# Kernel optimization log

Measured on AMD Instinct MI355X. Metric: run time of the kernel, lower is better.

The kernel has to match this reference:

```python
import jax, jax.numpy as jnp
import numpy as np

PATCH_SIDE = 20  # hardcoded in GenericCamera.project


def _resize_ac(img, out_h, out_w):
    """Bilinear resize with align_corners=True, matching F.interpolate. img: (B,C,H,W)."""
    B, C, H, W = img.shape
    ys = jnp.arange(out_h, dtype=jnp.float32) * (np.float32(H - 1) / np.float32(out_h - 1))
    xs = jnp.arange(out_w, dtype=jnp.float32) * (np.float32(W - 1) / np.float32(out_w - 1))
    y0 = jnp.floor(ys).astype(jnp.int32); y1 = jnp.minimum(y0 + 1, H - 1)
    x0 = jnp.floor(xs).astype(jnp.int32); x1 = jnp.minimum(x0 + 1, W - 1)
    wy = (ys - y0.astype(jnp.float32)).astype(img.dtype)
    wx = (xs - x0.astype(jnp.float32)).astype(img.dtype)
    top = img[:, :, y0, :] * (1 - wy)[None, None, :, None] + img[:, :, y1, :] * wy[None, None, :, None]
    return top[:, :, :, x0] * (1 - wx) + top[:, :, :, x1] * wx


def setup_inputs() -> dict:
    key = jax.random.key(0)
    k1, k2 = jax.random.split(key)
    B, H, W = 1, 128, 416
    R = jax.random.normal(k1, (B, 3, H, W), dtype=jnp.float32)
    X = jax.random.normal(k2, (B, 3, H, W), dtype=jnp.float32)
    return {"R": R, "X": X, "progress": 10}


def reference(R, X, progress):
    B, C, H_full, W_full = X.shape
    kh = PATCH_SIDE
    Ks = 2 * kh + 1          # 41
    K = Ks * Ks              # 1681
    H, W = H_full // 2, W_full // 2  # downsample=True

    ray = _resize_ac(R, H, W)          # (1,3,H,W)
    direction = _resize_ac(X, H, W)    # (1,3,H,W)

    # clamped patch window start per row/col (boundary shift logic of _get_patch_coords)
    sx = jnp.clip(jnp.arange(H) - kh, 0, H - 1 - 2 * kh)   # (H,)
    sy = jnp.clip(jnp.arange(W) - kh, 0, W - 1 - 2 * kh)   # (W,)
    off = jnp.arange(Ks)
    cx = sx[:, None] + off[None, :]    # (H,41) row indices of patch
    cy = sy[:, None] + off[None, :]    # (W,41) col indices of patch

    # separable patch gather: (3,H,W) -> (3,H,41,W) -> (3,H,41,W,41)
    r = ray[0]
    patch = r[:, cx, :][:, :, :, cy]                       # (3,H,41,W,41)
    patch = patch.transpose(0, 1, 3, 2, 4).reshape(3, H * W, K)  # (3,N,K)

    dirn = direction.reshape(B, 3, H * W)
    dirn = dirn / jnp.linalg.norm(dirn, axis=1, keepdims=True)
    d = dirn[0]                                            # (3,N)

    logits = jnp.einsum('cn,cnk->nk', d, patch)            # (N,K)
    temperature = np.float32(max(1e-8, 1e-4 / np.exp(0.1 * float(progress))))
    sm = jax.nn.softmax(logits / temperature, axis=-1)     # (N,K)

    # soft-argmax over patch coordinates (coords stored as (x,y) = (row,col))
    px = jnp.broadcast_to(cx[:, None, :, None], (H, W, Ks, Ks)).reshape(H * W, K).astype(jnp.float32)
    py = jnp.broadcast_to(cy[None, :, None, :], (H, W, Ks, Ks)).reshape(H * W, K).astype(jnp.float32)
    ix = jnp.einsum('nk,nk->n', sm, px).reshape(H, W)
    iy = jnp.einsum('nk,nk->n', sm, py).reshape(H, W)

    Xn = 2.0 * ix / (H - 1) - 1.0
    Yn = 2.0 * iy / (W - 1) - 1.0
    Xn = _resize_ac(Xn[None, None], H_full, W_full)[0, 0]
    Yn = _resize_ac(Yn[None, None], H_full, W_full)[0, 0]
    return jnp.stack([Yn, Xn], axis=-1).reshape(B, H_full, W_full, 2)
```

## Files before the change

kernel.cpp:

```cpp
#include <hip/hip_runtime.h>
#include <math.h>

#define HS 64
#define WS 208
#define HF 128
#define WF 416
#define NS (HS * WS)
#define KH 20
#define KS 41
#define KK (KS * KS)
#define NJ2 7
#define GRID 2048
#define LOG2E 1.442695040888963f

__device__ __forceinline__ void ac_idx(int o, int inN, float sc, int& i0, int& i1, float& w) {
#pragma clang fp contract(off)
    float s = (float)o * sc;
    float f = floorf(s);
    i0 = (int)f;
    i1 = min(i0 + 1, inN - 1);
    w = s - f;
}

__global__ void k_down(const float* __restrict__ R, const float* __restrict__ X,
                       const int* __restrict__ prog,
                       float4* __restrict__ ray4, float4* __restrict__ dir4,
                       float* __restrict__ tbuf) {
#pragma clang fp contract(off)
    int n = blockIdx.x * blockDim.x + threadIdx.x;
    if (n >= NS) return;
    if (n == 0) {
        double T64 = fmax(1e-8, 1e-4 / exp(0.1 * (double)prog[0]));
        tbuf[0] = (float)T64;
    }
    int y = n / WS, x = n - y * WS;
    int y0, y1, x0, x1; float wy, wx;
    ac_idx(y, HF, 127.0f / 63.0f, y0, y1, wy);
    ac_idx(x, WF, 415.0f / 207.0f, x0, x1, wx);
    float omwy = 1.0f - wy, omwx = 1.0f - wx;
    float r[3], d[3];
#pragma unroll
    for (int c = 0; c < 3; ++c) {
        const float* p = R + c * (HF * WF);
        float v00 = p[y0 * WF + x0], v10 = p[y1 * WF + x0];
        float v01 = p[y0 * WF + x1], v11 = p[y1 * WF + x1];
        float a0 = v00 * omwy; float b0 = v10 * wy; float t0 = a0 + b0;
        float a1 = v01 * omwy; float b1 = v11 * wy; float t1 = a1 + b1;
        float c0 = t0 * omwx; float c1 = t1 * wx;
        r[c] = c0 + c1;
        const float* q = X + c * (HF * WF);
        float u00 = q[y0 * WF + x0], u10 = q[y1 * WF + x0];
        float u01 = q[y0 * WF + x1], u11 = q[y1 * WF + x1];
        float e0 = u00 * omwy; float f0 = u10 * wy; float s0 = e0 + f0;
        float e1 = u01 * omwy; float f1 = u11 * wy; float s1 = e1 + f1;
        float g0 = s0 * omwx; float g1 = s1 * wx;
        d[c] = g0 + g1;
    }
    float q0 = d[0] * d[0]; float q1 = d[1] * d[1]; float q2 = d[2] * d[2];
    float ssq = (q0 + q1) + q2;
    float nrm = (float)sqrt((double)ssq);
    ray4[n] = make_float4(r[0], r[1], r[2], 0.0f);
    dir4[n] = make_float4(d[0] / nrm, d[1] / nrm, d[2] / nrm, 0.0f);
}

__global__ __launch_bounds__(256, 6) void k_main(const float4* __restrict__ ray4,
                                                 const float4* __restrict__ dir4,
                                                 const float* __restrict__ tbuf,
                                                 float* __restrict__ xn,
                                                 float* __restrict__ yn) {
#pragma clang fp contract(off)
    int tid = (int)threadIdx.x;
    int lane = tid & 63;
    int wid = tid >> 6;
    int k1i = (tid * 25) >> 10;
    int k2i = tid - k1i * KS;
    float Tf = tbuf[0];

    __shared__ float smax[4];
    __shared__ float ssum[4][3];

    for (int pix = (int)blockIdx.x; pix < NS; pix += GRID) {
        int h = pix / WS, w = pix - h * WS;
        int srow = min(max(h - KH, 0), HS - 1 - 2 * KH);
        int scol = min(max(w - KH, 0), WS - 1 - 2 * KH);

        float4 dv = dir4[pix];
        float d0 = dv.x, d1 = dv.y, d2 = dv.z;

        int off = (srow + k1i) * WS + scol + k2i;
        int colk = k2i;

        float lg[NJ2];
        float m = -INFINITY;
#pragma unroll
        for (int j = 0; j < NJ2 - 1; ++j) {
            float4 v = ray4[off];
            float p0 = d0 * v.x; float p1 = d1 * v.y; float p2 = d2 * v.z;
            float l = (p0 + p1) + p2;
            lg[j] = l;
            m = fmaxf(m, l);
            int cn = colk + 10;
            bool cr = cn >= KS;
            colk = cr ? cn - KS : cn;
            off += cr ? (7 * WS - 31) : (6 * WS + 10);
        }
        {
            float l = -INFINITY;
            if (tid < KK - 256 * (NJ2 - 1)) {
                float4 v = ray4[off];
                float p0 = d0 * v.x; float p1 = d1 * v.y; float p2 = d2 * v.z;
                l = (p0 + p1) + p2;
            }
            lg[NJ2 - 1] = l;
            m = fmaxf(m, l);
        }
#pragma unroll
        for (int s = 1; s < 64; s <<= 1) m = fmaxf(m, __shfl_xor(m, s));

        if (lane == 0) smax[wid] = m;
        __syncthreads();
        m = fmaxf(fmaxf(smax[0], smax[1]), fmaxf(smax[2], smax[3]));

        float zm = m / Tf;
        float thresh = m - 0.004f;

        float se = 0.f, sr = 0.f, sc = 0.f;
        int c1 = k1i, c2 = k2i;
#pragma unroll
        for (int j = 0; j < NJ2; ++j) {
            bool a = lg[j] > thresh;
            if (__ballot(a)) {
                float z = lg[j] / Tf;
                float arg = (z - zm) * LOG2E;
                float e = a ? __builtin_amdgcn_exp2f(arg) : 0.0f;
                se += e;
                sr += e * (float)(srow + c1);
                sc += e * (float)(scol + c2);
            }
            int cn = c2 + 10;
            bool cr = cn >= KS;
            c2 = cr ? cn - KS : cn;
            c1 += cr ? 7 : 6;
        }
#pragma unroll
        for (int s = 1; s < 64; s <<= 1) {
            se += __shfl_xor(se, s);
            sr += __shfl_xor(sr, s);
            sc += __shfl_xor(sc, s);
        }
        if (lane == 0) { ssum[wid][0] = se; ssum[wid][1] = sr; ssum[wid][2] = sc; }
        __syncthreads();
        if (tid == 0) {
            float SE = (ssum[0][0] + ssum[1][0]) + (ssum[2][0] + ssum[3][0]);
            float SR = (ssum[0][1] + ssum[1][1]) + (ssum[2][1] + ssum[3][1]);
            float SC = (ssum[0][2] + ssum[1][2]) + (ssum[2][2] + ssum[3][2]);
            double ix = (double)SR / (double)SE, iy = (double)SC / (double)SE;
            xn[pix] = (float)(2.0 * ix / (double)(HS - 1) - 1.0);
            yn[pix] = (float)(2.0 * iy / (double)(WS - 1) - 1.0);
        }
    }
}

__global__ void k_up(const float* __restrict__ xn, const float* __restrict__ yn,
                     float* __restrict__ out) {
#pragma clang fp contract(off)
    int i = blockIdx.x * blockDim.x + threadIdx.x;
    if (i >= HF * WF) return;
    int hh = i / WF, ww = i - hh * WF;
    int y0, y1, x0, x1; float wy, wx;
    ac_idx(hh, HS, 63.0f / 127.0f, y0, y1, wy);
    ac_idx(ww, WS, 207.0f / 415.0f, x0, x1, wx);
    float omwy = 1.0f - wy, omwx = 1.0f - wx;
    float a0, b0, t0, t1;
    a0 = xn[y0 * WS + x0] * omwy; b0 = xn[y1 * WS + x0] * wy; t0 = a0 + b0;
    a0 = xn[y0 * WS + x1] * omwy; b0 = xn[y1 * WS + x1] * wy; t1 = a0 + b0;
    float bx = t0 * omwx + t1 * wx;
    a0 = yn[y0 * WS + x0] * omwy; b0 = yn[y1 * WS + x0] * wy; t0 = a0 + b0;
    a0 = yn[y0 * WS + x1] * omwy; b0 = yn[y1 * WS + x1] * wy; t1 = a0 + b0;
    float ay = t0 * omwx + t1 * wx;
    out[2 * i]     = ay;
    out[2 * i + 1] = bx;
}

extern "C" void kernel_launch(void* const* d_in, const int* in_sizes, int n_in,
                              void* d_out, int out_size, void* d_ws, size_t ws_size,
                              hipStream_t stream) {
    const float* R = (const float*)d_in[0];
    const float* X = (const float*)d_in[1];
    const int* prog = (const int*)d_in[2];
    float4* ray4 = (float4*)d_ws;
    float4* dir4 = ray4 + NS;
    float* xn   = (float*)(dir4 + NS);
    float* yn   = xn + NS;
    float* tbuf = yn + NS;
    float* out  = (float*)d_out;

    k_down<<<(NS + 255) / 256, 256, 0, stream>>>(R, X, prog, ray4, dir4, tbuf);
    k_main<<<GRID, 256, 0, stream>>>(ray4, dir4, tbuf, xn, yn);
    k_up<<<(HF * WF + 255) / 256, 256, 0, stream>>>(xn, yn, out);
}
```

Baseline: 33.33 us.

## Share a staged LDS patch tile across eight pixels, one wave per pixel

Replaces the per-pixel 256-thread block (grid-stride over pixels) with blocks of 512 threads that handle eight horizontally adjacent pixels of one row. The union of their 41x48 patch window is loaded cooperatively into shared memory once. Each wave then computes one pixel's softmax soft-argmax from LDS with only wave-level shuffles, removing block barriers per pixel and redundant global/L2 reads of overlapping patches. It trades this for 31KB of LDS per block and more serial work per lane (27 elements). The ray buffer is padded because the tile load can read past the end of the array.

```diff
diff --git a/kernel.cpp b/kernel.cpp
--- a/kernel.cpp
+++ b/kernel.cpp
@@ -9,8 +9,10 @@
 #define KH 20
 #define KS 41
 #define KK (KS * KS)
-#define NJ2 7
-#define GRID 2048
+#define TCOL 48
+#define PITCH 49
+#define TEL (KS * TCOL)
+#define NBLK (HS * 26)
 #define LOG2E 1.442695040888963f
 
 __device__ __forceinline__ void ac_idx(int o, int inN, float sc, int& i0, int& i1, float& w) {
@@ -63,101 +65,106 @@
     dir4[n] = make_float4(d[0] / nrm, d[1] / nrm, d[2] / nrm, 0.0f);
 }
 
-__global__ __launch_bounds__(256, 6) void k_main(const float4* __restrict__ ray4,
-                                                 const float4* __restrict__ dir4,
-                                                 const float* __restrict__ tbuf,
-                                                 float* __restrict__ xn,
-                                                 float* __restrict__ yn) {
-#pragma clang fp contract(off)
-    int tid = (int)threadIdx.x;
-    int lane = tid & 63;
-    int wid = tid >> 6;
-    int k1i = (tid * 25) >> 10;
-    int k2i = tid - k1i * KS;
+__global__ __launch_bounds__(512) void k_oct(const float4* __restrict__ ray4,
+                                             const float4* __restrict__ dir4,
+                                             const float* __restrict__ tbuf,
+                                             float* __restrict__ xn,
+                                             float* __restrict__ yn) {
+#pragma clang fp contract(off)
+    __shared__ float4 tile[KS * PITCH];
+    int t = (int)threadIdx.x;
+    int lane = t & 63;
+    int wv = t >> 6;
+    int blk = (int)blockIdx.x;
+    int row = (blk * 2521) >> 16;
+    int grp = blk - row * 26;
+    int w0 = grp * 8;
+    int srow = min(max(row - KH, 0), HS - 1 - 2 * KH);
+    int scol0 = min(max(w0 - KH, 0), WS - 1 - 2 * KH);
+
+    int base = srow * WS + scol0;
+#pragma unroll
+    for (int s = 0; s < 4; ++s) {
+        int e = t + 512 * s;
+        if (e < TEL) {
+            int i = (e * 683) >> 15;
+            int j = e - i * TCOL;
+            tile[i * PITCH + j] = ray4[base + i * WS + j];
+        }
+    }
+    __syncthreads();
+
+    int wpx = w0 + wv;
+    int scolp = min(max(wpx - KH, 0), WS - 1 - 2 * KH);
+    int dJ = scolp - scol0;
+    float4 dv = dir4[row * WS + wpx];
+    float d0 = dv.x, d1 = dv.y, d2 = dv.z;
     float Tf = tbuf[0];
 
-    __shared__ float smax[4];
-    __shared__ float ssum[4][3];
-
-    for (int pix = (int)blockIdx.x; pix < NS; pix += GRID) {
-        int h = pix / WS, w = pix - h * WS;
-        int srow = min(max(h - KH, 0), HS - 1 - 2 * KH);
-        int scol = min(max(w - KH, 0), WS - 1 - 2 * KH);
-
-        float4 dv = dir4[pix];
-        float d0 = dv.x, d1 = dv.y, d2 = dv.z;
-
-        int off = (srow + k1i) * WS + scol + k2i;
-        int colk = k2i;
-
-        float lg[NJ2];
-        float m = -INFINITY;
-#pragma unroll
-        for (int j = 0; j < NJ2 - 1; ++j) {
-            float4 v = ray4[off];
+    int k1i = (lane * 25) >> 10;
+    int k2i = lane - k1i * KS;
+    int loff = k1i * PITCH + dJ + k2i;
+    int colk = k2i;
+
+    float lg[27];
+    float m = -INFINITY;
+#pragma unroll
+    for (int j = 0; j < 26; ++j) {
+        float4 v = tile[loff];
+        float p0 = d0 * v.x; float p1 = d1 * v.y; float p2 = d2 * v.z;
+        float l = (p0 + p1) + p2;
+        lg[j] = l;
+        m = fmaxf(m, l);
+        int cn = colk + 23;
+        bool cr = cn >= KS;
+        colk = cr ? cn - KS : cn;
+        loff += cr ? (2 * PITCH - 18) : (PITCH + 23);
+    }
+    {
+        float l = -INFINITY;
+        if (lane < KK - 64 * 26) {
+            float4 v = tile[loff];
             float p0 = d0 * v.x; float p1 = d1 * v.y; float p2 = d2 * v.z;
-            float l = (p0 + p1) + p2;
-            lg[j] = l;
-            m = fmaxf(m, l);
-            int cn = colk + 10;
-            bool cr = cn >= KS;
-            colk = cr ? cn - KS : cn;
-            off += cr ? (7 * WS - 31) : (6 * WS + 10);
+            l = (p0 + p1) + p2;
         }
-        {
-            float l = -INFINITY;
-            if (tid < KK - 256 * (NJ2 - 1)) {
-                float4 v = ray4[off];
-                float p0 = d0 * v.x; float p1 = d1 * v.y; float p2 = d2 * v.z;
-                l = (p0 + p1) + p2;
-            }
-            lg[NJ2 - 1] = l;
-            m = fmaxf(m, l);
+        lg[26] = l;
+        m = fmaxf(m, l);
+    }
+#pragma unroll
+    for (int s = 1; s < 64; s <<= 1) m = fmaxf(m, __shfl_xor(m, s));
+
+    float zm = m / Tf;
+    float thresh = m - 0.004f;
+
+    float se = 0.f, sr = 0.f, sc = 0.f;
+    int c1 = k1i, c2 = k2i;
+#pragma unroll
+    for (int j = 0; j < 27; ++j) {
+        bool a = lg[j] > thresh;
+        if (__ballot(a)) {
+            float z = lg[j] / Tf;
+            float arg = (z - zm) * LOG2E;
+            float e = a ? __builtin_amdgcn_exp2f(arg) : 0.0f;
+            se += e;
+            sr += e * (float)(srow + c1);
+            sc += e * (float)(scolp + c2);
         }
-#pragma unroll
-        for (int s = 1; s < 64; s <<= 1) m = fmaxf(m, __shfl_xor(m, s));
-
-        if (lane == 0) smax[wid] = m;
-        __syncthreads();
-        m = fmaxf(fmaxf(smax[0], smax[1]), fmaxf(smax[2], smax[3]));
-
-        float zm = m / Tf;
-        float thresh = m - 0.004f;
-
-        float se = 0.f, sr = 0.f, sc = 0.f;
-        int c1 = k1i, c2 = k2i;
-#pragma unroll
-        for (int j = 0; j < NJ2; ++j) {
-            bool a = lg[j] > thresh;
-            if (__ballot(a)) {
-                float z = lg[j] / Tf;
-                float arg = (z - zm) * LOG2E;
-                float e = a ? __builtin_amdgcn_exp2f(arg) : 0.0f;
-                se += e;
-                sr += e * (float)(srow + c1);
-                sc += e * (float)(scol + c2);
-            }
-            int cn = c2 + 10;
-            bool cr = cn >= KS;
-            c2 = cr ? cn - KS : cn;
-            c1 += cr ? 7 : 6;
-        }
-#pragma unroll
-        for (int s = 1; s < 64; s <<= 1) {
-            se += __shfl_xor(se, s);
-            sr += __shfl_xor(sr, s);
-            sc += __shfl_xor(sc, s);
-        }
-        if (lane == 0) { ssum[wid][0] = se; ssum[wid][1] = sr; ssum[wid][2] = sc; }
-        __syncthreads();
-        if (tid == 0) {
-            float SE = (ssum[0][0] + ssum[1][0]) + (ssum[2][0] + ssum[3][0]);
-            float SR = (ssum[0][1] + ssum[1][1]) + (ssum[2][1] + ssum[3][1]);
-            float SC = (ssum[0][2] + ssum[1][2]) + (ssum[2][2] + ssum[3][2]);
-            double ix = (double)SR / (double)SE, iy = (double)SC / (double)SE;
-            xn[pix] = (float)(2.0 * ix / (double)(HS - 1) - 1.0);
-            yn[pix] = (float)(2.0 * iy / (double)(WS - 1) - 1.0);
-        }
+        int cn = c2 + 23;
+        bool cr = cn >= KS;
+        c2 = cr ? cn - KS : cn;
+        c1 += cr ? 2 : 1;
+    }
+#pragma unroll
+    for (int s = 1; s < 64; s <<= 1) {
+        se += __shfl_xor(se, s);
+        sr += __shfl_xor(sr, s);
+        sc += __shfl_xor(sc, s);
+    }
+    if (lane == 0) {
+        int pix = row * WS + wpx;
+        double ix = (double)sr / (double)se, iy = (double)sc / (double)se;
+        xn[pix] = (float)(2.0 * ix / (double)(HS - 1) - 1.0);
+        yn[pix] = (float)(2.0 * iy / (double)(WS - 1) - 1.0);
     }
 }
 
@@ -189,13 +196,13 @@
     const float* X = (const float*)d_in[1];
     const int* prog = (const int*)d_in[2];
     float4* ray4 = (float4*)d_ws;
-    float4* dir4 = ray4 + NS;
+    float4* dir4 = ray4 + NS + 8;
     float* xn   = (float*)(dir4 + NS);
     float* yn   = xn + NS;
     float* tbuf = yn + NS;
     float* out  = (float*)d_out;
 
     k_down<<<(NS + 255) / 256, 256, 0, stream>>>(R, X, prog, ray4, dir4, tbuf);
-    k_main<<<GRID, 256, 0, stream>>>(ray4, dir4, tbuf, xn, yn);
+    k_oct<<<NBLK, 512, 0, stream>>>(ray4, dir4, tbuf, xn, yn);
     k_up<<<(HF * WF + 255) / 256, 256, 0, stream>>>(xn, yn, out);
 }
```

Measured after the change: 36.85 us. 1.11x slower.
